# Kernel tuning notes

Measured on AMD Instinct MI355X. Metric: run time of the kernel, lower is better.

Reference implementation:

```python
import jax, jax.numpy as jnp
import numpy as np

B, NX, NH, NY, K = 4096, 512, 512, 256, 8


def setup_inputs() -> dict:
    key = jax.random.key(0)
    k0, k1, k2, k3, k4, k5 = jax.random.split(key, 6)
    s = 1.0 / np.sqrt(NH)  # torch RNNCell init scale
    x = jax.random.normal(k0, (B, NX), jnp.float32)
    h = jax.random.normal(k1, (B, NH), jnp.float32)
    pi = jax.random.uniform(k2, (B, K), jnp.float32)
    pi = pi / pi.sum(axis=1, keepdims=True)  # __init_belief normalizes to sum 1
    W_ih = jax.random.uniform(k3, (K, NH, NX), jnp.float32, minval=-s, maxval=s)
    W_hh = jax.random.uniform(k4, (K, NH, NH), jnp.float32, minval=-s, maxval=s)
    W_out = jax.random.uniform(k5, (NY, NH), jnp.float32, minval=-s, maxval=s)
    return {"x": x, "h": h, "pi": pi, "W_ih": W_ih, "W_hh": W_hh, "W_out": W_out}


def reference(x, h, pi, W_ih, W_hh, W_out):
    # Per-state RNN cells (bias=False): h_k[:, :, k] = tanh(x @ W_ih[k].T + h @ W_hh[k].T)
    h_k = jnp.tanh(
        jnp.einsum('bx,knx->bnk', x, W_ih)
        + jnp.einsum('bh,knh->bnk', h, W_hh)
    )  # (B, NH, K)
    # out_k = out_layer applied per state: (B, NY, K)
    out_k = jnp.einsum('bnk,yn->byk', h_k, W_out)
    # belief-weighted soft combination of hidden states: states[b] = h_k[b] @ pi[b]
    h_mix = jnp.einsum('bnk,bk->bn', h_k, pi)  # (B, NH)
    out = h_mix @ W_out.T  # (B, NY)
    return (out, h_mix, out_k, h_k)
```

## Files before the change

kernel.cpp:

```cpp
#include <hip/hip_runtime.h>
#include <hip/hip_bf16.h>
#include <stdint.h>

typedef unsigned short u16;
typedef __attribute__((ext_vector_type(8))) short short8;
typedef __attribute__((ext_vector_type(4))) float f32x4;

#define BATCH 4096
#define OFF_OUT  0
#define OFF_HMIX (BATCH * 256)
#define OFF_OK   (OFF_HMIX + BATCH * 512)
#define OFF_HK   (OFF_OK + BATCH * 256 * 8)

#define WS_XB   0
#define WS_HB   (2097152)
#define WS_WIH  (4194304)
#define WS_WHH  (6291456)
#define WS_WOUT (8388608)
#define WS_T    (8519680)
#define WS_OB   (25296896)

__device__ __forceinline__ float b2f(u16 v) {
  union { uint32_t u; float f; } c; c.u = ((uint32_t)v) << 16; return c.f;
}
__device__ __forceinline__ u16 f2b(float f) {
  union { float f; uint32_t u; } c; c.f = f;
  uint32_t u = c.u;
  return (u16)((u + 0x7fffu + ((u >> 16) & 1u)) >> 16);
}

__device__ __forceinline__ void gload16(const u16* g, u16* l) {
  __builtin_amdgcn_global_load_lds(
      (const __attribute__((address_space(1))) void*)g,
      (__attribute__((address_space(3))) void*)l, 16, 0, 0);
}

__global__ __launch_bounds__(256) void k0_cvt(
    const float* __restrict__ x, const float* __restrict__ h,
    const float* __restrict__ Wih, const float* __restrict__ Whh,
    const float* __restrict__ Wout, u16* __restrict__ ws) {
  const int i = blockIdx.x * 256 + threadIdx.x;
  const float* src; int j; size_t dst;
  if      (i <  524288) { src = x;    j = i;           dst = WS_XB;   }
  else if (i < 1048576) { src = h;    j = i -  524288; dst = WS_HB;   }
  else if (i < 1572864) { src = Wih;  j = i - 1048576; dst = WS_WIH;  }
  else if (i < 2097152) { src = Whh;  j = i - 1572864; dst = WS_WHH;  }
  else                  { src = Wout; j = i - 2097152; dst = WS_WOUT; }
  const float4 v = ((const float4*)src)[j];
  ushort4 o;
  o.x = f2b(v.x); o.y = f2b(v.y); o.z = f2b(v.z); o.w = f2b(v.w);
  ((ushort4*)(ws + dst))[j] = o;
}

__global__ __launch_bounds__(512, 2) void k1_gemm_tanh(
    const u16* __restrict__ xb, const u16* __restrict__ hb,
    const u16* __restrict__ Wih, const u16* __restrict__ Whh,
    u16* __restrict__ Tb) {
  __shared__ u16 S[65536];
  const int tid  = threadIdx.x;
  const int lane = tid & 63;
  const int w    = tid >> 6;
  const int wm   = w >> 2;
  const int wn   = w & 3;
  const int quad = lane >> 4, rl = lane & 15, l7 = lane & 7;
  const int sr   = tid >> 3;
  const int sc   = ((tid & 7) ^ (sr & 7)) * 8;

  const int wg  = blockIdx.x;
  const int lin = ((wg & 7) << 5) | (wg >> 3);
  const int bx  = lin & 15;
  const int by  = lin >> 4;
  const int row0 = bx * 256;
  const int col0 = by * 256;
  const int kk   = col0 >> 9;
  const int nh0  = col0 & 511;

  const u16* const As2[2] = { xb, hb };
  const u16* const Bs2[2] = { Wih + (size_t)kk * 262144, Whh + (size_t)kk * 262144 };

  auto stage = [&](int tile, int region) {
    if (tile >= 16) return;
    const int g    = tile >> 3;
    const int ko   = (tile & 7) * 64;
    const int isB  = region >> 1;
    const int half = region & 1;
    const u16* src = isB ? Bs2[g] : As2[g];
    const int r0   = (isB ? nh0 : row0) + half * 128;
    u16* dst = S + (tile & 1) * 32768 + isB * 16384 + half * 8192;
    const u16* s0 = src + (size_t)(r0 + sr) * 512 + ko + sc;
    gload16(s0,            dst + tid * 8);
    gload16(s0 + 64 * 512, dst + 4096 + tid * 8);
  };

  auto ldA = [&](int buf, int mi, int ks) -> short8 {
    return *(const short8*)&S[buf * 32768 +
                              (wm * 128 + mi * 16 + rl) * 64 +
                              ((ks * 4 + quad) ^ l7) * 8];
  };
  auto ldB = [&](int buf, int j, int ks) -> short8 {
    return *(const short8*)&S[buf * 32768 + 16384 +
                              (wn * 64 + j * 16 + rl) * 64 +
                              ((ks * 4 + quad) ^ l7) * 8];
  };

  f32x4 acc[8][4] = {};

  stage(0, 0); stage(0, 1); stage(0, 2); stage(0, 3);
  stage(1, 0); stage(1, 1);
  asm volatile("s_waitcnt vmcnt(4)" ::: "memory");
  __builtin_amdgcn_s_barrier();
  asm volatile("" ::: "memory");

#pragma unroll 1
  for (int t = 0; t < 16; ++t) {
    const int buf = t & 1;
    short8 al[4][2], ah[4][2], bf[4][2];

#pragma unroll
    for (int m = 0; m < 4; ++m) { al[m][0] = ldA(buf, m, 0); al[m][1] = ldA(buf, m, 1); }
#pragma unroll
    for (int j = 0; j < 4; ++j) { bf[j][0] = ldB(buf, j, 0); bf[j][1] = ldB(buf, j, 1); }
    stage(t + 1, 2);
    stage(t + 1, 3);

    __builtin_amdgcn_s_setprio(1);
#pragma unroll
    for (int m = 0; m < 4; ++m)
#pragma unroll
      for (int n = 0; n < 4; ++n)
#pragma unroll
        for (int ks = 0; ks < 2; ++ks)
          acc[m][n] = __builtin_amdgcn_mfma_f32_16x16x32_bf16(al[m][ks], bf[n][ks], acc[m][n], 0, 0, 0);
    __builtin_amdgcn_s_setprio(0);

#pragma unroll
    for (int m = 0; m < 4; ++m) { ah[m][0] = ldA(buf, 4 + m, 0); ah[m][1] = ldA(buf, 4 + m, 1); }

    __builtin_amdgcn_s_setprio(1);
#pragma unroll
    for (int m = 0; m < 4; ++m)
#pragma unroll
      for (int n = 2; n < 4; ++n)
#pragma unroll
        for (int ks = 0; ks < 2; ++ks)
          acc[4 + m][n] = __builtin_amdgcn_mfma_f32_16x16x32_bf16(ah[m][ks], bf[n][ks], acc[4 + m][n], 0, 0, 0);
    __builtin_amdgcn_s_setprio(0);

    asm volatile("s_waitcnt lgkmcnt(0)" ::: "memory");
    __builtin_amdgcn_s_barrier();
    stage(t + 2, 0);
    stage(t + 2, 1);

    __builtin_amdgcn_s_setprio(1);
#pragma unroll
    for (int m = 0; m < 4; ++m)
#pragma unroll
      for (int n = 0; n < 2; ++n)
#pragma unroll
        for (int ks = 0; ks < 2; ++ks)
          acc[4 + m][n] = __builtin_amdgcn_mfma_f32_16x16x32_bf16(ah[m][ks], bf[n][ks], acc[4 + m][n], 0, 0, 0);
    __builtin_amdgcn_s_setprio(0);

    if (t < 14) asm volatile("s_waitcnt vmcnt(4)" ::: "memory");
    else        asm volatile("s_waitcnt vmcnt(0)" ::: "memory");
    __builtin_amdgcn_s_barrier();
    asm volatile("" ::: "memory");
  }

#pragma unroll 1
  for (int hp = 0; hp < 2; ++hp) {
    if (wm == hp) {
#pragma unroll
      for (int m = 0; m < 8; ++m)
#pragma unroll
        for (int n = 0; n < 4; ++n)
#pragma unroll
          for (int r = 0; r < 4; ++r) {
            const int lr = m * 16 + quad * 4 + r;
            const float v = acc[m][n][r];
            const float e = __expf(2.0f * v);
            S[lr * 264 + wn * 64 + n * 16 + rl] = f2b(1.0f - 2.0f / (e + 1.0f));
          }
    }
    asm volatile("s_waitcnt lgkmcnt(0)" ::: "memory");
    __builtin_amdgcn_s_barrier();
#pragma unroll
    for (int p = 0; p < 8; ++p) {
      const int idx = p * 512 + tid;
      const int c = idx & 31, rr = idx >> 5;
      *(short8*)&Tb[(size_t)(row0 + hp * 128 + rr) * 4096 + col0 + c * 8] =
          *(const short8*)&S[rr * 264 + c * 8];
    }
    __builtin_amdgcn_s_barrier();
  }
}

__global__ __launch_bounds__(256) void k2_gemm_out(
    const u16* __restrict__ Tb, const u16* __restrict__ Wout,
    u16* __restrict__ Ob) {
  __shared__ u16 S[128 * 136];
  u16* As = S;
  u16* Bs = S + 128 * 64;
  const int tid  = threadIdx.x;
  const int lane = tid & 63;
  const int w    = tid >> 6;
  const int wm   = w >> 1, wn = w & 1;
  const int row0 = blockIdx.x * 128;
  const int y0   = blockIdx.y * 128;
  const int kk   = blockIdx.z;
  const int sr   = tid >> 3;
  const int sc   = ((tid & 7) ^ ((tid >> 3) & 7)) * 8;
  const int ldsw = (w * 8) * 64;

  f32x4 acc[4][4] = {};

  for (int kt = 0; kt < 8; ++kt) {
    const int kb = kt * 64;
#pragma unroll
    for (int ro = 0; ro < 4; ++ro) {
      gload16(Tb + (size_t)(row0 + ro * 32 + sr) * 4096 + kk * 512 + kb + sc,
              &As[ro * 32 * 64 + ldsw]);
      gload16(Wout + (size_t)(y0 + ro * 32 + sr) * 512 + kb + sc,
              &Bs[ro * 32 * 64 + ldsw]);
    }
    __syncthreads();
    const int l7 = lane & 7, quad = lane >> 4, rl = lane & 15;
#pragma unroll
    for (int ks = 0; ks < 2; ++ks) {
      short8 af[4], bf[4];
      const int cs = ((ks * 4 + quad) ^ l7) * 8;
#pragma unroll
      for (int i = 0; i < 4; ++i)
        af[i] = *(const short8*)&As[(wm * 64 + i * 16 + rl) * 64 + cs];
#pragma unroll
      for (int j = 0; j < 4; ++j)
        bf[j] = *(const short8*)&Bs[(wn * 64 + j * 16 + rl) * 64 + cs];
#pragma unroll
      for (int i = 0; i < 4; ++i)
#pragma unroll
        for (int j = 0; j < 4; ++j)
          acc[i][j] = __builtin_amdgcn_mfma_f32_16x16x32_bf16(af[i], bf[j], acc[i][j], 0, 0, 0);
    }
    __syncthreads();
  }

  const int quad = lane >> 4, cl = lane & 15;
#pragma unroll
  for (int i = 0; i < 4; ++i)
#pragma unroll
    for (int j = 0; j < 4; ++j)
#pragma unroll
      for (int r = 0; r < 4; ++r) {
        const int row = wm * 64 + i * 16 + quad * 4 + r;
        const int col = wn * 64 + j * 16 + cl;
        S[row * 136 + col] = f2b(acc[i][j][r]);
      }
  __syncthreads();
#pragma unroll
  for (int it = 0; it < 8; ++it) {
    const int idx = it * 256 + tid;
    const int c = idx & 15;
    const int r = idx >> 4;
    *(short8*)&Ob[(size_t)(row0 + r) * 2048 + kk * 256 + y0 + c * 8] =
        *(const short8*)&S[r * 136 + c * 8];
  }
}

__global__ __launch_bounds__(512) void k3_epi(const float* __restrict__ pi,
                                              const u16* __restrict__ Tb,
                                              const u16* __restrict__ Ob,
                                              float* __restrict__ dout) {
  const int b   = blockIdx.x;
  const int tid = threadIdx.x;

  float pif[8];
#pragma unroll
  for (int k = 0; k < 8; ++k) pif[k] = pi[b * 8 + k];

  float tv[8]; float hm = 0.0f;
#pragma unroll
  for (int k = 0; k < 8; ++k) {
    const float v = b2f(Tb[(size_t)b * 4096 + k * 512 + tid]);
    tv[k] = v; hm += pif[k] * v;
  }
  float4* tw = (float4*)&dout[OFF_HK + (size_t)b * 4096 + tid * 8];
  tw[0] = make_float4(tv[0], tv[1], tv[2], tv[3]);
  tw[1] = make_float4(tv[4], tv[5], tv[6], tv[7]);
  dout[OFF_HMIX + (size_t)b * 512 + tid] = hm;

  if (tid < 256) {
    float ov[8]; float om = 0.0f;
#pragma unroll
    for (int k = 0; k < 8; ++k) {
      const float v = b2f(Ob[(size_t)b * 2048 + k * 256 + tid]);
      ov[k] = v; om += pif[k] * v;
    }
    float4* ow = (float4*)&dout[OFF_OK + (size_t)b * 2048 + tid * 8];
    ow[0] = make_float4(ov[0], ov[1], ov[2], ov[3]);
    ow[1] = make_float4(ov[4], ov[5], ov[6], ov[7]);
    dout[OFF_OUT + (size_t)b * 256 + tid] = om;
  }
}

extern "C" void kernel_launch(void* const* d_in, const int* in_sizes, int n_in,
                              void* d_out, int out_size, void* d_ws, size_t ws_size,
                              hipStream_t stream) {
  const float* x    = (const float*)d_in[0];
  const float* h    = (const float*)d_in[1];
  const float* pi   = (const float*)d_in[2];
  const float* Wih  = (const float*)d_in[3];
  const float* Whh  = (const float*)d_in[4];
  const float* Wout = (const float*)d_in[5];
  float* out = (float*)d_out;
  u16* ws  = (u16*)d_ws;

  k0_cvt<<<dim3(8320), 256, 0, stream>>>(x, h, Wih, Whh, Wout, ws);
  k1_gemm_tanh<<<dim3(256), 512, 0, stream>>>(
      ws + WS_XB, ws + WS_HB, ws + WS_WIH, ws + WS_WHH, ws + WS_T);
  k2_gemm_out<<<dim3(32, 2, 8), 256, 0, stream>>>(ws + WS_T, ws + WS_WOUT, ws + WS_OB);
  k3_epi<<<dim3(BATCH), 512, 0, stream>>>(pi, ws + WS_T, ws + WS_OB, out);
}
```

Before: 211.5 us.

## Prefetch next tile's LDS fragments during last MFMA block of current tile

Restructures the GEMM main loop so the A low-half and B low-half fragments for the next K tile are read from LDS right after the barrier. Those reads overlap with the final MFMA quadrant of the current tile, which hides LDS read latency at the start of each iteration. The loop is unrolled by two with ping-pong B-fragment registers and the MFMA quadrants are reordered. The s_setprio hints are dropped. Register pressure rises from keeping extra fragments live, which risks lower occupancy or spills.

New measurement: 209.4 us. No clear change (-1.0%).

```diff
diff --git a/kernel.cpp b/kernel.cpp
--- a/kernel.cpp
+++ b/kernel.cpp
@@ -104,68 +104,93 @@
   };
 
   f32x4 acc[8][4] = {};
+  short8 al[4][2], ah[4][2], bh[2][2], blA[2][2], blB[2][2];
 
   stage(0, 0); stage(0, 1); stage(0, 2); stage(0, 3);
   stage(1, 0); stage(1, 1);
   asm volatile("s_waitcnt vmcnt(4)" ::: "memory");
   __builtin_amdgcn_s_barrier();
   asm volatile("" ::: "memory");
+#pragma unroll
+  for (int m = 0; m < 4; ++m) { al[m][0] = ldA(0, m, 0); al[m][1] = ldA(0, m, 1); }
+#pragma unroll
+  for (int j = 0; j < 2; ++j) { blA[j][0] = ldB(0, j, 0); blA[j][1] = ldB(0, j, 1); }
+
+#define TILE_BODY(T, BUF, BLc, BLn)                                            \
+  {                                                                            \
+                                         \
+    _Pragma("unroll")                                                          \
+    for (int j = 0; j < 2; ++j) {                                              \
+      bh[j][0] = ldB(BUF, 2 + j, 0); bh[j][1] = ldB(BUF, 2 + j, 1);            \
+    }                                                                          \
+    stage((T) + 1, 2); stage((T) + 1, 3);                                      \
+                           \
+    _Pragma("unroll")                                                          \
+    for (int m = 0; m < 4; ++m)                                                \
+      _Pragma("unroll")                                                        \
+      for (int n = 0; n < 2; ++n)                                              \
+        _Pragma("unroll")                                                      \
+        for (int ks = 0; ks < 2; ++ks)                                         \
+          acc[m][n] = __builtin_amdgcn_mfma_f32_16x16x32_bf16(                 \
+              al[m][ks], BLc[n][ks], acc[m][n], 0, 0, 0);                      \
+                                                        \
+    _Pragma("unroll")                                                          \
+    for (int m = 0; m < 4; ++m) {                                              \
+      ah[m][0] = ldA(BUF, 4 + m, 0); ah[m][1] = ldA(BUF, 4 + m, 1);            \
+    }                                                                          \
+                                                          \
+    _Pragma("unroll")                                                          \
+    for (int m = 0; m < 4; ++m)                                                \
+      _Pragma("unroll")                                                        \
+      for (int n = 0; n < 2; ++n)                                              \
+        _Pragma("unroll")                                                      \
+        for (int ks = 0; ks < 2; ++ks)                                         \
+          acc[m][2 + n] = __builtin_amdgcn_mfma_f32_16x16x32_bf16(             \
+              al[m][ks], bh[n][ks], acc[m][2 + n], 0, 0, 0);                   \
+                                      \
+    asm volatile("s_waitcnt lgkmcnt(0)" ::: "memory");                         \
+    __builtin_amdgcn_s_barrier();                                              \
+    stage((T) + 2, 0); stage((T) + 2, 1);                                      \
+                                                          \
+    _Pragma("unroll")                                                          \
+    for (int m = 0; m < 4; ++m)                                                \
+      _Pragma("unroll")                                                        \
+      for (int n = 0; n < 2; ++n)                                              \
+        _Pragma("unroll")                                                      \
+        for (int ks = 0; ks < 2; ++ks)                                         \
+          acc[4 + m][2 + n] = __builtin_amdgcn_mfma_f32_16x16x32_bf16(         \
+              ah[m][ks], bh[n][ks], acc[4 + m][2 + n], 0, 0, 0);               \
+                 \
+    if ((T) < 14) asm volatile("s_waitcnt vmcnt(4)" ::: "memory");             \
+    else          asm volatile("s_waitcnt vmcnt(0)" ::: "memory");             \
+    __builtin_amdgcn_s_barrier();                                              \
+    asm volatile("" ::: "memory");                                             \
+        \
+    _Pragma("unroll")                                                          \
+    for (int m = 0; m < 4; ++m) {                                              \
+      al[m][0] = ldA(1 - (BUF), m, 0); al[m][1] = ldA(1 - (BUF), m, 1);        \
+    }                                                                          \
+    _Pragma("unroll")                                                          \
+    for (int j = 0; j < 2; ++j) {                                              \
+      BLn[j][0] = ldB(1 - (BUF), j, 0); BLn[j][1] = ldB(1 - (BUF), j, 1);      \
+    }                                                                          \
+                                         \
+    _Pragma("unroll")                                                          \
+    for (int m = 0; m < 4; ++m)                                                \
+      _Pragma("unroll")                                                        \
+      for (int n = 0; n < 2; ++n)                                              \
+        _Pragma("unroll")                                                      \
+        for (int ks = 0; ks < 2; ++ks)                                         \
+          acc[4 + m][n] = __builtin_amdgcn_mfma_f32_16x16x32_bf16(             \
+              ah[m][ks], BLc[n][ks], acc[4 + m][n], 0, 0, 0);                  \
+  }
 
 #pragma unroll 1
-  for (int t = 0; t < 16; ++t) {
-    const int buf = t & 1;
-    short8 al[4][2], ah[4][2], bf[4][2];
-
-#pragma unroll
-    for (int m = 0; m < 4; ++m) { al[m][0] = ldA(buf, m, 0); al[m][1] = ldA(buf, m, 1); }
-#pragma unroll
-    for (int j = 0; j < 4; ++j) { bf[j][0] = ldB(buf, j, 0); bf[j][1] = ldB(buf, j, 1); }
-    stage(t + 1, 2);
-    stage(t + 1, 3);
-
-    __builtin_amdgcn_s_setprio(1);
-#pragma unroll
-    for (int m = 0; m < 4; ++m)
-#pragma unroll
-      for (int n = 0; n < 4; ++n)
-#pragma unroll
-        for (int ks = 0; ks < 2; ++ks)
-          acc[m][n] = __builtin_amdgcn_mfma_f32_16x16x32_bf16(al[m][ks], bf[n][ks], acc[m][n], 0, 0, 0);
-    __builtin_amdgcn_s_setprio(0);
-
-#pragma unroll
-    for (int m = 0; m < 4; ++m) { ah[m][0] = ldA(buf, 4 + m, 0); ah[m][1] = ldA(buf, 4 + m, 1); }
-
-    __builtin_amdgcn_s_setprio(1);
-#pragma unroll
-    for (int m = 0; m < 4; ++m)
-#pragma unroll
-      for (int n = 2; n < 4; ++n)
-#pragma unroll
-        for (int ks = 0; ks < 2; ++ks)
-          acc[4 + m][n] = __builtin_amdgcn_mfma_f32_16x16x32_bf16(ah[m][ks], bf[n][ks], acc[4 + m][n], 0, 0, 0);
-    __builtin_amdgcn_s_setprio(0);
-
-    asm volatile("s_waitcnt lgkmcnt(0)" ::: "memory");
-    __builtin_amdgcn_s_barrier();
-    stage(t + 2, 0);
-    stage(t + 2, 1);
-
-    __builtin_amdgcn_s_setprio(1);
-#pragma unroll
-    for (int m = 0; m < 4; ++m)
-#pragma unroll
-      for (int n = 0; n < 2; ++n)
-#pragma unroll
-        for (int ks = 0; ks < 2; ++ks)
-          acc[4 + m][n] = __builtin_amdgcn_mfma_f32_16x16x32_bf16(ah[m][ks], bf[n][ks], acc[4 + m][n], 0, 0, 0);
-    __builtin_amdgcn_s_setprio(0);
-
-    if (t < 14) asm volatile("s_waitcnt vmcnt(4)" ::: "memory");
-    else        asm volatile("s_waitcnt vmcnt(0)" ::: "memory");
-    __builtin_amdgcn_s_barrier();
-    asm volatile("" ::: "memory");
-  }
+  for (int tp = 0; tp < 8; ++tp) {
+    TILE_BODY(2 * tp,     0, blA, blB);
+    TILE_BODY(2 * tp + 1, 1, blB, blA);
+  }
+#undef TILE_BODY
 
 #pragma unroll 1
   for (int hp = 0; hp < 2; ++hp) {
```
